# Performance work log

Hardware: AMD Instinct MI355X
Metric: run time of the kernel (lower is better)

Reference implementation:

```python
import jax, jax.numpy as jnp
import numpy as np

H, W = 100, 100  # local_env_shape


def setup_inputs() -> dict:
    key = jax.random.key(0)
    k1, = jax.random.split(key, 1)
    B, T, P = 32, 10, 25
    # points in [0, 110): with resolution=1, origin=0 most land in the 100x100 grid,
    x = jax.random.uniform(k1, (B, T, 2 * P), dtype=jnp.float32) * 110.0
    resolution = jnp.ones((B, T, 2), dtype=jnp.float32)
    origin = jnp.zeros((B, T, 2), dtype=jnp.float32)
    return {"x": x, "resolution": resolution, "origin": origin}


def reference(x, resolution, origin):
    B, T, n = x.shape
    P = n // 2
    points = x.reshape(B, T, P, 2)  # [B, T, P, 2] (x, y)
    # row index from y-coordinate, col index from x-coordinate (cast truncates, as tf.cast does)
    row = (points[..., 1] / resolution[:, :, 0:1] + origin[:, :, 0:1]).astype(jnp.int32)  # [B,T,P]
    col = (points[..., 0] / resolution[:, :, 1:2] + origin[:, :, 1:2]).astype(jnp.int32)  # [B,T,P]
    in_bounds = (row >= 0) & (row < H) & (col >= 0) & (col < W)  # [B,T,P]
    row_safe = jnp.clip(row, 0, H - 1)
    col_safe = jnp.clip(col, 0, W - 1)
    b_idx = jnp.arange(B)[:, None, None]
    t_idx = jnp.arange(T)[None, :, None]
    p_idx = jnp.arange(P)[None, None, :]
    grid = jnp.zeros((B, T, H, W, P), dtype=jnp.float32)
    # scatter-max so masked-out (OOB) points write 0 and never clobber a valid 1
    out = grid.at[b_idx, t_idx, row_safe, col_safe, p_idx].max(in_bounds.astype(jnp.float32))
    return out
```

## Files before the change

kernel.cpp:

```cpp
#include <hip/hip_runtime.h>

#define BB 32
#define TT 10
#define PP 25
#define HH 100
#define WW 100

#define N4_PER_BT ((HH * WW * PP) / 4)
#define BLOCKS_PER_BT 8

typedef float f32x4 __attribute__((ext_vector_type(4)));

__global__ __launch_bounds__(256) void raster_dense_kernel(
        const float* __restrict__ x,
        const float* __restrict__ resolution,
        const float* __restrict__ origin,
        float* __restrict__ out) {
    const int bt  = blockIdx.y;
    const int tid = threadIdx.x;

    __shared__ int cell[PP];
    if (tid < PP) {
        const float px = x[bt * (2 * PP) + 2 * tid];
        const float py = x[bt * (2 * PP) + 2 * tid + 1];
        const float r0 = resolution[bt * 2 + 0];
        const float r1 = resolution[bt * 2 + 1];
        const float o0 = origin[bt * 2 + 0];
        const float o1 = origin[bt * 2 + 1];
        const int row = (int)(py / r0 + o0);
        const int col = (int)(px / r1 + o1);
        cell[tid] = (row >= 0 && row < HH && col >= 0 && col < WW)
                        ? (row * WW + col) : -1;
    }
    __syncthreads();

    float* const base = out + (size_t)bt * (HH * WW * PP);

    for (int i4 = blockIdx.x * 256 + tid; i4 < N4_PER_BT;
         i4 += BLOCKS_PER_BT * 256) {
        const int e  = i4 * 4;
        int hw = e / PP;
        int p  = e - hw * PP;

        f32x4 v;
#pragma unroll
        for (int j = 0; j < 4; ++j) {
            v[j] = (cell[p] == hw) ? 1.0f : 0.0f;
            if (++p == PP) { p = 0; ++hw; }
        }

        __builtin_nontemporal_store(
            v, reinterpret_cast<f32x4*>(base + e));
    }
}

extern "C" void kernel_launch(void* const* d_in, const int* in_sizes, int n_in,
                              void* d_out, int out_size, void* d_ws, size_t ws_size,
                              hipStream_t stream) {
    const float* x          = (const float*)d_in[0];
    const float* resolution = (const float*)d_in[1];
    const float* origin     = (const float*)d_in[2];
    float* out = (float*)d_out;

    dim3 grid(BLOCKS_PER_BT, BB * TT);
    raster_dense_kernel<<<grid, 256, 0, stream>>>(x, resolution, origin, out);
}
```

Baseline: 317.5 us.

## Zero-fill output segments then scatter ones for in-bounds points per segment

Replaces the dense per-element compare with a plain zero fill of each block's contiguous segment, followed by a barrier and a sparse write of 1.0 for points whose cell falls in that segment. It also drops the nontemporal store hint and uses a 1D grid of 10 blocks per (b,t). This removes per-element index math and shared-memory compares, so the kernel becomes a pure store stream. The risk is that regular stores instead of nontemporal ones may pollute cache, and the scatter adds a small tail after the barrier.

```diff
diff --git a/kernel.cpp b/kernel.cpp
--- a/kernel.cpp
+++ b/kernel.cpp
@@ -6,20 +6,35 @@
 #define HH 100
 #define WW 100
 
-#define N4_PER_BT ((HH * WW * PP) / 4)
-#define BLOCKS_PER_BT 8
+#define CELLS (HH * WW)
+#define ELEMS_PER_BT (CELLS * PP)
+#define BLOCKS_PER_BT 10
+#define F4_PER_BLOCK 6250
+#define CELLS_PER_BLOCK (CELLS / BLOCKS_PER_BT)
 
 typedef float f32x4 __attribute__((ext_vector_type(4)));
 
-__global__ __launch_bounds__(256) void raster_dense_kernel(
+__global__ __launch_bounds__(256) void raster_zero_fixup_kernel(
         const float* __restrict__ x,
         const float* __restrict__ resolution,
         const float* __restrict__ origin,
         float* __restrict__ out) {
-    const int bt  = blockIdx.y;
+    const int bid = blockIdx.x;
     const int tid = threadIdx.x;
+    const int bt  = bid / BLOCKS_PER_BT;
+    const int seg = bid % BLOCKS_PER_BT;
 
-    __shared__ int cell[PP];
+    float* const chunk =
+        out + (size_t)bt * ELEMS_PER_BT + (size_t)seg * (F4_PER_BLOCK * 4);
+
+    const f32x4 z = {0.0f, 0.0f, 0.0f, 0.0f};
+#pragma unroll 4
+    for (int i = tid; i < F4_PER_BLOCK; i += 256) {
+        reinterpret_cast<f32x4*>(chunk)[i] = z;
+    }
+
+    __syncthreads();
+
     if (tid < PP) {
         const float px = x[bt * (2 * PP) + 2 * tid];
         const float py = x[bt * (2 * PP) + 2 * tid + 1];
@@ -29,28 +44,13 @@
         const float o1 = origin[bt * 2 + 1];
         const int row = (int)(py / r0 + o0);
         const int col = (int)(px / r1 + o1);
-        cell[tid] = (row >= 0 && row < HH && col >= 0 && col < WW)
-                        ? (row * WW + col) : -1;
-    }
-    __syncthreads();
-
-    float* const base = out + (size_t)bt * (HH * WW * PP);
-
-    for (int i4 = blockIdx.x * 256 + tid; i4 < N4_PER_BT;
-         i4 += BLOCKS_PER_BT * 256) {
-        const int e  = i4 * 4;
-        int hw = e / PP;
-        int p  = e - hw * PP;
-
-        f32x4 v;
-#pragma unroll
-        for (int j = 0; j < 4; ++j) {
-            v[j] = (cell[p] == hw) ? 1.0f : 0.0f;
-            if (++p == PP) { p = 0; ++hw; }
+        if (row >= 0 && row < HH && col >= 0 && col < WW) {
+            const int cellIdx = row * WW + col;
+            const int lo = seg * CELLS_PER_BLOCK;
+            if (cellIdx >= lo && cellIdx < lo + CELLS_PER_BLOCK) {
+                out[(size_t)bt * ELEMS_PER_BT + (size_t)cellIdx * PP + tid] = 1.0f;
+            }
         }
-
-        __builtin_nontemporal_store(
-            v, reinterpret_cast<f32x4*>(base + e));
     }
 }
 
@@ -62,6 +62,7 @@
     const float* origin     = (const float*)d_in[2];
     float* out = (float*)d_out;
 
-    dim3 grid(BLOCKS_PER_BT, BB * TT);
-    raster_dense_kernel<<<grid, 256, 0, stream>>>(x, resolution, origin, out);
+    const int nblocks = BB * TT * BLOCKS_PER_BT;
+    raster_zero_fixup_kernel<<<nblocks, 256, 0, stream>>>(x, resolution, origin,
+                                                          out);
 }
```

Result: slower. 326.8 us (+2.9%).
